# Optimization experiments

Measured on AMD Instinct MI355X. Metric: run time of the kernel, lower is better.

## Reference

```python
import jax, jax.numpy as jnp
import numpy as np

N = 50000   # nodes
E = 800000  # edges (before self-loops)
D = 96      # hidden_dim (= per-head out_channels, concat=False averages heads)
H = 4       # heads
L = 2       # num_layers
NEG_SLOPE = 0.2
EPS_BN = 1e-5


def setup_inputs() -> dict:
    key = jax.random.key(0)
    ks = jax.random.split(key, 8)
    x = jax.random.normal(ks[0], (N, D), dtype=jnp.float32)
    edge_index = jax.random.randint(ks[1], (2, E), 0, N, dtype=jnp.int64)
    # GATConv shared lin: in D -> H*D (per-head dim D), Glorot-ish scale
    W = jax.random.normal(ks[2], (L, D, H * D), dtype=jnp.float32) / np.sqrt(D).astype(np.float32)
    att_src = jax.random.normal(ks[3], (L, H, D), dtype=jnp.float32) * 0.1
    att_dst = jax.random.normal(ks[4], (L, H, D), dtype=jnp.float32) * 0.1
    bias = jnp.zeros((L, D), dtype=jnp.float32)
    gamma = jnp.ones((L, D), dtype=jnp.float32)
    beta = jnp.zeros((L, D), dtype=jnp.float32)
    return dict(x=x, edge_index=edge_index, W=W, att_src=att_src,
                att_dst=att_dst, bias=bias, gamma=gamma, beta=beta)


def _gat_layer(x, src, dst, W, a_src, a_dst, b):
    h = (x @ W).reshape(N, H, D)                      # [N,H,D]
    alpha_src = jnp.einsum('nhd,hd->nh', h, a_src)    # [N,H]
    alpha_dst = jnp.einsum('nhd,hd->nh', h, a_dst)    # [N,H]
    e = jax.nn.leaky_relu(alpha_src[src] + alpha_dst[dst], NEG_SLOPE)  # [Etot,H]
    # edge softmax grouped by destination node (numerically stable)
    m = jax.ops.segment_max(e, dst, num_segments=N)   # [N,H]
    p = jnp.exp(e - m[dst])
    denom = jax.ops.segment_sum(p, dst, num_segments=N)
    alpha = p / (denom[dst] + 1e-16)                  # [Etot,H]
    msg = h[src] * alpha[:, :, None]                  # [Etot,H,D]
    out = jax.ops.segment_sum(msg, dst, num_segments=N)  # [N,H,D]
    return out.mean(axis=1) + b                       # concat=False -> head mean


def reference(x, edge_index, W, att_src, att_dst, bias, gamma, beta):
    # PyG GATConv adds self-loops by default
    loops = jnp.arange(N, dtype=edge_index.dtype)
    ei = jnp.concatenate([edge_index, jnp.stack([loops, loops])], axis=1)
    src, dst = ei[0], ei[1]
    for l in range(L):
        x_res = x
        out = _gat_layer(x, src, dst, W[l], att_src[l], att_dst[l], bias[l])
        # BatchNorm over nodes (training-mode batch statistics, biased var)
        mu = out.mean(axis=0)
        var = out.var(axis=0)
        out = (out - mu) / jnp.sqrt(var + EPS_BN) * gamma[l] + beta[l]
        # dropout is identity at inference
        x = jax.nn.relu(out) + x_res
    return x
```

## Files before the change

### kernel.cpp

```cpp
#include <hip/hip_runtime.h>

#define DD 96
#define HH 4
#define HD 384
#define NEG_SLOPE 0.2f
#define NB_STATS 128
#define SCAN_BS 1024
#define WTC 400

typedef unsigned int uint;
typedef unsigned short ushort;
typedef __attribute__((ext_vector_type(8))) short bf16x8;
typedef __attribute__((ext_vector_type(4))) float f32x4;

__device__ inline uint pack2bf(float lo, float hi) {
    uint ulo = __float_as_uint(lo); ulo += 0x7fffu + ((ulo >> 16) & 1u);
    uint uhi = __float_as_uint(hi); uhi += 0x7fffu + ((uhi >> 16) & 1u);
    return (ulo >> 16) | (uhi & 0xffff0000u);
}
__device__ inline ushort f2bf(float f) {
    uint u = __float_as_uint(f);
    u += 0x7fffu + ((u >> 16) & 1u);
    return (ushort)(u >> 16);
}

__global__ void wa_kernel(const float* __restrict__ W, const float* __restrict__ att_src,
                          const float* __restrict__ att_dst, float* __restrict__ wa) {
    const int l = blockIdx.x / DD;
    const int k = blockIdx.x % DD;
    const int t = threadIdx.x;
    const float* Wr = W + ((size_t)l * DD + k) * HD;
    const float* as = att_src + (size_t)l * HD;
    const float* ad = att_dst + (size_t)l * HD;
    const bool hiHalf = t >= 32;
    float s0=0,s1=0,s2=0,s3=0,d0=0,d1=0,d2=0,d3=0;
    int c; float w, ps, pd;
    c = t;       w = Wr[c]; s0 = fmaf(w, as[c], s0); d0 = fmaf(w, ad[c], d0);
    c = t + 64;  w = Wr[c]; ps = w * as[c]; pd = w * ad[c];
    s0 += hiHalf ? 0.f : ps;  s1 += hiHalf ? ps : 0.f;
    d0 += hiHalf ? 0.f : pd;  d1 += hiHalf ? pd : 0.f;
    c = t + 128; w = Wr[c]; s1 = fmaf(w, as[c], s1); d1 = fmaf(w, ad[c], d1);
    c = t + 192; w = Wr[c]; s2 = fmaf(w, as[c], s2); d2 = fmaf(w, ad[c], d2);
    c = t + 256; w = Wr[c]; ps = w * as[c]; pd = w * ad[c];
    s2 += hiHalf ? 0.f : ps;  s3 += hiHalf ? ps : 0.f;
    d2 += hiHalf ? 0.f : pd;  d3 += hiHalf ? pd : 0.f;
    c = t + 320; w = Wr[c]; s3 = fmaf(w, as[c], s3); d3 = fmaf(w, ad[c], d3);
#pragma unroll
    for (int off = 32; off; off >>= 1) {
        s0 += __shfl_xor(s0, off); s1 += __shfl_xor(s1, off);
        s2 += __shfl_xor(s2, off); s3 += __shfl_xor(s3, off);
        d0 += __shfl_xor(d0, off); d1 += __shfl_xor(d1, off);
        d2 += __shfl_xor(d2, off); d3 += __shfl_xor(d3, off);
    }
    if (t == 0) {
        float* o = wa + ((size_t)l * DD + k) * 8;
        o[0]=s0; o[1]=d0; o[2]=s1; o[3]=d1; o[4]=s2; o[5]=d2; o[6]=s3; o[7]=d3;
    }
}

__global__ void wt_kernel(const float* __restrict__ W, const float* __restrict__ wa,
                          ushort* __restrict__ wt) {
    const int l = blockIdx.x / WTC;
    const int c = blockIdx.x % WTC;
    const int k = threadIdx.x;
    float v = 0.f;
    if (c < HD)        v = W[((size_t)l * DD + k) * HD + c];
    else if (c < HD+8) v = wa[((size_t)l * DD + k) * 8 + (c - HD)];
    wt[((size_t)l * WTC + c) * DD + k] = f2bf(v);
}

template<int FUSE>
__global__ void __launch_bounds__(256) gemm_mfma_kernel(const float* __restrict__ xin,
        const float* __restrict__ scsh, const float* __restrict__ xres,
        float* __restrict__ xout,
        const ushort* __restrict__ wt, uint* __restrict__ hp,
        float* __restrict__ asrc, float* __restrict__ adst, int N) {
    const int t = threadIdx.x;
    const int w = t >> 6;
    const int lane = t & 63;
    const int q = lane & 15, g = lane >> 4;
    const int base = blockIdx.x * 64 + w * 16;
    const int nA = min(base + q, N - 1);

    f32x4 acc[25];
#pragma unroll
    for (int i = 0; i < 25; i++) acc[i] = (f32x4){0.f, 0.f, 0.f, 0.f};

#pragma unroll
    for (int s = 0; s < 3; s++) {
        const int kbase = s * 32 + g * 8;
        float xv[8];
        if (FUSE == 0) {
            const float* xp = xin + (size_t)nA * DD + kbase;
            const float4 xa = *(const float4*)xp;
            const float4 xb = *(const float4*)(xp + 4);
            xv[0]=xa.x; xv[1]=xa.y; xv[2]=xa.z; xv[3]=xa.w;
            xv[4]=xb.x; xv[5]=xb.y; xv[6]=xb.z; xv[7]=xb.w;
        } else {
            const float* yp = xin + (size_t)nA * DD + kbase;
            const float* rp = xres + (size_t)nA * DD + kbase;
            const float4 ya = *(const float4*)yp;
            const float4 yb = *(const float4*)(yp + 4);
            const float4 ra = *(const float4*)rp;
            const float4 rb = *(const float4*)(rp + 4);
            const float yv[8] = {ya.x,ya.y,ya.z,ya.w,yb.x,yb.y,yb.z,yb.w};
            const float rv[8] = {ra.x,ra.y,ra.z,ra.w,rb.x,rb.y,rb.z,rb.w};
#pragma unroll
            for (int j = 0; j < 8; j++) {
                const int d = kbase + j;
                float a = fmaf(yv[j], scsh[d], scsh[d + DD]);
                xv[j] = (a > 0.f ? a : 0.f) + rv[j];
            }
            float* op = xout + (size_t)nA * DD + kbase;
            *(float4*)op       = make_float4(xv[0], xv[1], xv[2], xv[3]);
            *(float4*)(op + 4) = make_float4(xv[4], xv[5], xv[6], xv[7]);
        }
        union { uint u[4]; bf16x8 v; } A;
        A.u[0] = pack2bf(xv[0], xv[1]);
        A.u[1] = pack2bf(xv[2], xv[3]);
        A.u[2] = pack2bf(xv[4], xv[5]);
        A.u[3] = pack2bf(xv[6], xv[7]);
#pragma unroll
        for (int tt = 0; tt < 25; tt++) {
            const ushort* wp = wt + (size_t)(tt * 16 + q) * DD + kbase;
            union { uint4 u4; bf16x8 v; } B;
            B.u4 = *(const uint4*)wp;
            acc[tt] = __builtin_amdgcn_mfma_f32_16x16x32_bf16(A.v, B.v, acc[tt], 0, 0, 0);
        }
    }
#pragma unroll
    for (int r = 0; r < 4; r++) {
        const int node = base + g * 4 + r;
        if (node < N) {
            uint* hr = hp + (size_t)node * 192;
#pragma unroll
            for (int p = 0; p < 3; p++)
#pragma unroll
                for (int tt = 0; tt < 4; tt++)
                    hr[p * 64 + tt * 16 + q] = pack2bf(acc[p * 8 + tt][r], acc[p * 8 + tt + 4][r]);
            if (q < 8) {
                const float v = acc[24][r];
                if ((q & 1) == 0) asrc[node * 4 + (q >> 1)] = v;
                else              adst[node * 4 + (q >> 1)] = v;
            }
        }
    }
}

__global__ void count_kernel(const int* __restrict__ ei, int* __restrict__ deg, int E) {
    int i = blockIdx.x * blockDim.x + threadIdx.x;
    const int stride = gridDim.x * blockDim.x;
    for (; i < E; i += stride) atomicAdd(&deg[ei[E + i]], 1);
}

__global__ void scan1_kernel(const int* __restrict__ deg, int* __restrict__ locpre,
                             int* __restrict__ bsum, int N) {
    __shared__ int ts[256];
    const int t = threadIdx.x;
    const int base = blockIdx.x * SCAN_BS + t * 4;
    int e0 = 0, e1 = 0, e2 = 0, e3 = 0;
    if (base + 3 < N) {
        const int4 v = *(const int4*)(deg + base);
        e0 = v.x + 1; e1 = v.y + 1; e2 = v.z + 1; e3 = v.w + 1;
    } else {
        if (base     < N) e0 = deg[base]     + 1;
        if (base + 1 < N) e1 = deg[base + 1] + 1;
        if (base + 2 < N) e2 = deg[base + 2] + 1;
        if (base + 3 < N) e3 = deg[base + 3] + 1;
    }
    const int s = e0 + e1 + e2 + e3;
    ts[t] = s;
    __syncthreads();
    for (int off = 1; off < 256; off <<= 1) {
        const int u = (t >= off) ? ts[t - off] : 0;
        __syncthreads();
        ts[t] += u;
        __syncthreads();
    }
    const int ex = ts[t] - s;
    if (base + 3 < N) {
        *(int4*)(locpre + base) = make_int4(ex, ex + e0, ex + e0 + e1, ex + e0 + e1 + e2);
    } else if (base < N) {
        locpre[base] = ex;
        if (base + 1 < N) locpre[base + 1] = ex + e0;
        if (base + 2 < N) locpre[base + 2] = ex + e0 + e1;
    }
    if (t == 255) bsum[blockIdx.x] = ts[255];
}

__global__ void scan3_kernel(const int* __restrict__ locpre, const int* __restrict__ bsum,
                             int* __restrict__ rowptr, int* __restrict__ cursor,
                             int N, int NBLK) {
    __shared__ int s_boff, s_total;
    const int t = threadIdx.x;
    if (t < 64) {
        const int mine = (t < NBLK) ? bsum[t] : 0;
        int incl = mine;
#pragma unroll
        for (int off = 1; off < 64; off <<= 1) {
            const int u = __shfl_up(incl, off);
            if (t >= off) incl += u;
        }
        if (t == (int)blockIdx.x) s_boff = incl - mine;
        if (t == NBLK - 1) s_total = incl;
    }
    __syncthreads();
    const int boff = s_boff;
    const int base = blockIdx.x * SCAN_BS + t * 4;
    if (base + 3 < N) {
        int4 v = *(const int4*)(locpre + base);
        v.x += boff; v.y += boff; v.z += boff; v.w += boff;
        *(int4*)(rowptr + base) = v;
        *(int4*)(cursor + base) = v;
    } else {
        for (int i = base; i < N && i < base + 4; i++) {
            const int r = locpre[i] + boff;
            rowptr[i] = r; cursor[i] = r;
        }
    }
    if (blockIdx.x == 0 && t == 0) rowptr[N] = s_total;
}

__global__ void scatter_kernel(const int* __restrict__ ei, int* __restrict__ cursor,
                               const int* __restrict__ rowptr, int* __restrict__ col,
                               int E, int Etot) {
    int i = blockIdx.x * blockDim.x + threadIdx.x;
    const int stride = gridDim.x * blockDim.x;
    for (; i < Etot; i += stride) {
        if (i < E) {
            const int src = ei[i], dst = ei[E + i];
            col[atomicAdd(&cursor[dst], 1)] = src;
        } else {
            const int n = i - E;
            col[rowptr[n + 1] - 1] = n;
        }
    }
}

#define EDGE_FMA(u0, u1, u2, w4)                                                      \
    { den0 += w4.x; den1 += w4.y; den2 += w4.z; den3 += w4.w;                         \
      const float cf1 = hi32 ? w4.y : w4.x;                                           \
      const float cf4 = hi32 ? w4.w : w4.z;                                           \
      acc0 = fmaf(__uint_as_float(u0 << 16), w4.x, acc0);                             \
      acc1 = fmaf(__uint_as_float(u0 & 0xffff0000u), cf1, acc1);                      \
      acc2 = fmaf(__uint_as_float(u1 << 16), w4.y, acc2);                             \
      acc3 = fmaf(__uint_as_float(u1 & 0xffff0000u), w4.z, acc3);                     \
      acc4 = fmaf(__uint_as_float(u2 << 16), cf4, acc4);                              \
      acc5 = fmaf(__uint_as_float(u2 & 0xffff0000u), w4.w, acc5); }

__global__ void __launch_bounds__(256) agg_csr_kernel(
        const int* __restrict__ rowptr, const int* __restrict__ col,
        const uint* __restrict__ hp, const float* __restrict__ asrc,
        const float* __restrict__ adst, const float* __restrict__ bias,
        float* __restrict__ y, int N) {
    __shared__ float4 wls[4][64];
    __shared__ int    sls[4][64];
    const int t = threadIdx.x;
    const int lane = t & 63;
    const int wv = t >> 6;
    const bool hi32 = lane >= 32;
    const int n = (blockIdx.x * blockDim.x + t) >> 6;
    if (n >= N) return;
    const int beg = rowptr[n], endp = rowptr[n + 1];
    const float4 adv = ((const float4*)adst)[n];
    float acc0=0,acc1=0,acc2=0,acc3=0,acc4=0,acc5=0;
    float den0=0,den1=0,den2=0,den3=0;

    for (int cs = beg; cs < endp; cs += 64) {
        const int cnt = min(64, endp - cs);
        if (lane < cnt) {
            const int s = col[cs + lane];
            const float4 av = ((const float4*)asrc)[s];
            float e0 = av.x + adv.x, e1 = av.y + adv.y;
            float e2 = av.z + adv.z, e3 = av.w + adv.w;
            e0 = e0 > 0.f ? e0 : NEG_SLOPE * e0;
            e1 = e1 > 0.f ? e1 : NEG_SLOPE * e1;
            e2 = e2 > 0.f ? e2 : NEG_SLOPE * e2;
            e3 = e3 > 0.f ? e3 : NEG_SLOPE * e3;
            sls[wv][lane] = s;
            wls[wv][lane] = make_float4(__expf(e0), __expf(e1), __expf(e2), __expf(e3));
        }
        __builtin_amdgcn_wave_barrier();
        int j = 0;
        for (; j + 4 <= cnt; j += 4) {
            const int4 sv = *(const int4*)&sls[wv][j];
            const float4 wA = wls[wv][j],     wB = wls[wv][j + 1];
            const float4 wC = wls[wv][j + 2], wD = wls[wv][j + 3];
            const uint* h0 = hp + (size_t)sv.x * 192 + lane;
            const uint* h1 = hp + (size_t)sv.y * 192 + lane;
            const uint* h2 = hp + (size_t)sv.z * 192 + lane;
            const uint* h3 = hp + (size_t)sv.w * 192 + lane;
            const uint u00 = h0[0], u01 = h0[64], u02 = h0[128];
            const uint u10 = h1[0], u11 = h1[64], u12 = h1[128];
            const uint u20 = h2[0], u21 = h2[64], u22 = h2[128];
            const uint u30 = h3[0], u31 = h3[64], u32 = h3[128];
            EDGE_FMA(u00, u01, u02, wA);
            EDGE_FMA(u10, u11, u12, wB);
            EDGE_FMA(u20, u21, u22, wC);
            EDGE_FMA(u30, u31, u32, wD);
        }
        for (; j < cnt; j++) {
            const int s0 = sls[wv][j];
            const float4 wA = wls[wv][j];
            const uint* h0 = hp + (size_t)s0 * 192 + lane;
            const uint u00 = h0[0], u01 = h0[64], u02 = h0[128];
            EDGE_FMA(u00, u01, u02, wA);
        }
        __builtin_amdgcn_wave_barrier();
    }
    const float r0 = 0.25f / (den0 + 1e-16f);
    const float r1 = 0.25f / (den1 + 1e-16f);
    const float r2 = 0.25f / (den2 + 1e-16f);
    const float r3 = 0.25f / (den3 + 1e-16f);
    const float rc1 = hi32 ? r1 : r0;
    const float rc4 = hi32 ? r3 : r2;
    const float A = acc0 * r0 + acc3 * r2;
    const float B = acc1 * rc1 + acc4 * rc4;
    const float C = acc2 * r1 + acc5 * r3;
    const float shB = __shfl_xor(B, 32);
    const float shC = __shfl_xor(C, 32);
    float* yr = y + (size_t)n * DD;
    yr[lane] = A + (hi32 ? shC : shB) + bias[lane];
    if (!hi32) yr[64 + lane] = B + shC + bias[64 + lane];
}

__global__ void bnstats_kernel(const float* __restrict__ y, float* __restrict__ pbuf,
                               int total4) {
    __shared__ float ps[384 * 4];
    __shared__ float qs[384 * 4];
    const int t = threadIdx.x;
    const int stride = gridDim.x * 384;
    float s0=0,s1=0,s2=0,s3=0,q0=0,q1=0,q2=0,q3=0;
    for (int i = blockIdx.x * 384 + t; i < total4; i += stride) {
        const float4 v = ((const float4*)y)[i];
        s0 += v.x; q0 = fmaf(v.x, v.x, q0);
        s1 += v.y; q1 = fmaf(v.y, v.y, q1);
        s2 += v.z; q2 = fmaf(v.z, v.z, q2);
        s3 += v.w; q3 = fmaf(v.w, v.w, q3);
    }
    ps[t*4+0]=s0; ps[t*4+1]=s1; ps[t*4+2]=s2; ps[t*4+3]=s3;
    qs[t*4+0]=q0; qs[t*4+1]=q1; qs[t*4+2]=q2; qs[t*4+3]=q3;
    __syncthreads();
    if (t < 192) {
        const int d = t % 96;
        const float* src = (t < 96) ? ps : qs;
        float r = 0.f;
#pragma unroll
        for (int m = 0; m < 16; m++) r += src[d + 96 * m];
        pbuf[blockIdx.x * 192 + t] = r;
    }
}

__global__ void bnfin_kernel(const float* __restrict__ pbuf, const float* __restrict__ gamma,
                             const float* __restrict__ beta, float* __restrict__ scsh, int N) {
    const int d = threadIdx.x;
    float s = 0.f, q = 0.f;
    for (int b = 0; b < NB_STATS; b++) {
        s += pbuf[b * 192 + d];
        q += pbuf[b * 192 + 96 + d];
    }
    const float invN = 1.f / (float)N;
    const float mu = s * invN;
    const float var = q * invN - mu * mu;
    const float sc = gamma[d] * rsqrtf(var + 1e-5f);
    scsh[d] = sc;
    scsh[d + DD] = beta[d] - mu * sc;
}

__global__ void bn_apply_kernel(const float* __restrict__ y, const float* __restrict__ scsh,
                                const float* __restrict__ xin, float* __restrict__ xout,
                                int total4) {
    int i = blockIdx.x * blockDim.x + threadIdx.x;
    const int stride = gridDim.x * blockDim.x;
    for (; i < total4; i += stride) {
        const int d4 = (i % 24) * 4;
        const float4 v = ((const float4*)y)[i];
        const float4 xi = ((const float4*)xin)[i];
        float4 o; float a;
        a = fmaf(v.x, scsh[d4],     scsh[d4 + DD]);     o.x = (a > 0.f ? a : 0.f) + xi.x;
        a = fmaf(v.y, scsh[d4 + 1], scsh[d4 + 1 + DD]); o.y = (a > 0.f ? a : 0.f) + xi.y;
        a = fmaf(v.z, scsh[d4 + 2], scsh[d4 + 2 + DD]); o.z = (a > 0.f ? a : 0.f) + xi.z;
        a = fmaf(v.w, scsh[d4 + 3], scsh[d4 + 3 + DD]); o.w = (a > 0.f ? a : 0.f) + xi.w;
        ((float4*)xout)[i] = o;
    }
}

extern "C" void kernel_launch(void* const* d_in, const int* in_sizes, int n_in,
                              void* d_out, int out_size, void* d_ws, size_t ws_size,
                              hipStream_t stream) {
    const float* x        = (const float*)d_in[0];
    const int*   ei       = (const int*)d_in[1];
    const float* W        = (const float*)d_in[2];
    const float* att_src  = (const float*)d_in[3];
    const float* att_dst  = (const float*)d_in[4];
    const float* bias     = (const float*)d_in[5];
    const float* gamma    = (const float*)d_in[6];
    const float* beta     = (const float*)d_in[7];
    float* out_final = (float*)d_out;

    const int N = in_sizes[0] / DD;
    const int E = in_sizes[1] / 2;
    const int Etot = E + N;
    const int NBLK = (N + SCAN_BS - 1) / SCAN_BS;

    char* ws = (char*)d_ws;
    size_t off = 0;
    auto alloc = [&](size_t bytes) -> void* {
        void* p = ws + off;
        off += (bytes + 255) & ~(size_t)255;
        return p;
    };
    uint*   hp     = (uint*)alloc((size_t)N * 192 * 4);
    float*  asrc   = (float*)alloc((size_t)N * HH * 4);
    float*  adst   = (float*)alloc((size_t)N * HH * 4);
    float*  y      = (float*)alloc((size_t)N * DD * 4);
    float*  xbuf   = (float*)alloc((size_t)N * DD * 4);
    float*  pbuf   = (float*)alloc((size_t)NB_STATS * 192 * 4);
    float*  scsh   = (float*)alloc(2 * DD * 4);
    float*  wa     = (float*)alloc(2 * DD * 8 * 4);
    ushort* wt     = (ushort*)alloc((size_t)2 * WTC * DD * 2);
    int*    deg    = (int*)alloc((size_t)N * 4);
    int*    locpre = (int*)alloc((size_t)N * 4);
    int*    bsum   = (int*)alloc(64 * 4);
    int*    rowptr = (int*)alloc((size_t)(N + 1) * 4);
    int*    cursor = (int*)alloc((size_t)N * 4);
    int*    colidx = (int*)alloc((size_t)Etot * 4);

    hipMemsetAsync(deg, 0, (size_t)N * 4, stream);
    count_kernel<<<1024, 256, 0, stream>>>(ei, deg, E);
    scan1_kernel<<<NBLK, 256, 0, stream>>>(deg, locpre, bsum, N);
    scan3_kernel<<<NBLK, 256, 0, stream>>>(locpre, bsum, rowptr, cursor, N, NBLK);
    scatter_kernel<<<1024, 256, 0, stream>>>(ei, cursor, rowptr, colidx, E, Etot);
    wa_kernel<<<2 * DD, 64, 0, stream>>>(W, att_src, att_dst, wa);
    wt_kernel<<<2 * WTC, DD, 0, stream>>>(W, wa, wt);

    gemm_mfma_kernel<0><<<(N + 63) / 64, 256, 0, stream>>>(
        x, nullptr, nullptr, nullptr, wt, hp, asrc, adst, N);
    agg_csr_kernel<<<(N * 64 + 255) / 256, 256, 0, stream>>>(
        rowptr, colidx, hp, asrc, adst, bias, y, N);
    bnstats_kernel<<<NB_STATS, 384, 0, stream>>>(y, pbuf, N * DD / 4);
    bnfin_kernel<<<1, DD, 0, stream>>>(pbuf, gamma, beta, scsh, N);

    gemm_mfma_kernel<1><<<(N + 63) / 64, 256, 0, stream>>>(
        y, scsh, x, xbuf, wt + (size_t)WTC * DD, hp, asrc, adst, N);
    agg_csr_kernel<<<(N * 64 + 255) / 256, 256, 0, stream>>>(
        rowptr, colidx, hp, asrc, adst, bias + DD, y, N);
    bnstats_kernel<<<NB_STATS, 384, 0, stream>>>(y, pbuf, N * DD / 4);
    bnfin_kernel<<<1, DD, 0, stream>>>(pbuf, gamma + DD, beta + DD, scsh, N);
    bn_apply_kernel<<<2048, 256, 0, stream>>>(y, scsh, xbuf, out_final, N * DD / 4);
}
```

Baseline: 396.3 us.

## Fuse BatchNorm statistics into aggregation kernel via block-reduced atomics

Each aggregation block reduces per-feature sums and sums of squares in shared memory and atomically adds them to a 192-float global buffer. This replaces the separate bnstats pass that re-read y, and the GEMM kernel zeroes the buffer beforehand. It saves one full read of the output and one launch per layer, at the cost of heavy atomic contention on 192 addresses and a sync in every aggregation block.

```diff
diff --git a/kernel.cpp b/kernel.cpp
--- a/kernel.cpp
+++ b/kernel.cpp
@@ -4,7 +4,6 @@
 #define HH 4
 #define HD 384
 #define NEG_SLOPE 0.2f
-#define NB_STATS 128
 #define SCAN_BS 1024
 #define WTC 400
 
@@ -72,7 +71,7 @@
 template<int FUSE>
 __global__ void __launch_bounds__(256) gemm_mfma_kernel(const float* __restrict__ xin,
         const float* __restrict__ scsh, const float* __restrict__ xres,
-        float* __restrict__ xout,
+        float* __restrict__ xout, float* __restrict__ bnsum,
         const ushort* __restrict__ wt, uint* __restrict__ hp,
         float* __restrict__ asrc, float* __restrict__ adst, int N) {
     const int t = threadIdx.x;
@@ -81,6 +80,7 @@
     const int q = lane & 15, g = lane >> 4;
     const int base = blockIdx.x * 64 + w * 16;
     const int nA = min(base + q, N - 1);
+    if (blockIdx.x == 0 && t < 192) bnsum[t] = 0.f;
 
     f32x4 acc[25];
 #pragma unroll
@@ -252,17 +252,20 @@
         const int* __restrict__ rowptr, const int* __restrict__ col,
         const uint* __restrict__ hp, const float* __restrict__ asrc,
         const float* __restrict__ adst, const float* __restrict__ bias,
-        float* __restrict__ y, int N) {
+        float* __restrict__ y, float* __restrict__ bnsum, int N) {
     __shared__ float4 wls[4][64];
     __shared__ int    sls[4][64];
+    __shared__ float  bsm[4][96];
+    __shared__ float  bsq[4][96];
     const int t = threadIdx.x;
     const int lane = t & 63;
     const int wv = t >> 6;
     const bool hi32 = lane >= 32;
     const int n = (blockIdx.x * blockDim.x + t) >> 6;
-    if (n >= N) return;
-    const int beg = rowptr[n], endp = rowptr[n + 1];
-    const float4 adv = ((const float4*)adst)[n];
+    const bool valid = n < N;
+    int beg = 0, endp = 0;
+    float4 adv = make_float4(0.f, 0.f, 0.f, 0.f);
+    if (valid) { beg = rowptr[n]; endp = rowptr[n + 1]; adv = ((const float4*)adst)[n]; }
     float acc0=0,acc1=0,acc2=0,acc3=0,acc4=0,acc5=0;
     float den0=0,den1=0,den2=0,den3=0;
 
@@ -319,49 +322,38 @@
     const float C = acc2 * r1 + acc5 * r3;
     const float shB = __shfl_xor(B, 32);
     const float shC = __shfl_xor(C, 32);
-    float* yr = y + (size_t)n * DD;
-    yr[lane] = A + (hi32 ? shC : shB) + bias[lane];
-    if (!hi32) yr[64 + lane] = B + shC + bias[64 + lane];
-}
-
-__global__ void bnstats_kernel(const float* __restrict__ y, float* __restrict__ pbuf,
-                               int total4) {
-    __shared__ float ps[384 * 4];
-    __shared__ float qs[384 * 4];
-    const int t = threadIdx.x;
-    const int stride = gridDim.x * 384;
-    float s0=0,s1=0,s2=0,s3=0,q0=0,q1=0,q2=0,q3=0;
-    for (int i = blockIdx.x * 384 + t; i < total4; i += stride) {
-        const float4 v = ((const float4*)y)[i];
-        s0 += v.x; q0 = fmaf(v.x, v.x, q0);
-        s1 += v.y; q1 = fmaf(v.y, v.y, q1);
-        s2 += v.z; q2 = fmaf(v.z, v.z, q2);
-        s3 += v.w; q3 = fmaf(v.w, v.w, q3);
-    }
-    ps[t*4+0]=s0; ps[t*4+1]=s1; ps[t*4+2]=s2; ps[t*4+3]=s3;
-    qs[t*4+0]=q0; qs[t*4+1]=q1; qs[t*4+2]=q2; qs[t*4+3]=q3;
+    float val0 = 0.f, val1 = 0.f;
+    if (valid) {
+        val0 = A + (hi32 ? shC : shB) + bias[lane];
+        val1 = B + shC + bias[64 + lane];
+        float* yr = y + (size_t)n * DD;
+        yr[lane] = val0;
+        if (!hi32) yr[64 + lane] = val1;
+    }
+    bsm[wv][lane] = val0;
+    bsq[wv][lane] = val0 * val0;
+    if (!hi32) {
+        const float v1 = valid ? val1 : 0.f;
+        bsm[wv][64 + lane] = v1;
+        bsq[wv][64 + lane] = v1 * v1;
+    }
     __syncthreads();
-    if (t < 192) {
-        const int d = t % 96;
-        const float* src = (t < 96) ? ps : qs;
-        float r = 0.f;
-#pragma unroll
-        for (int m = 0; m < 16; m++) r += src[d + 96 * m];
-        pbuf[blockIdx.x * 192 + t] = r;
-    }
-}
-
-__global__ void bnfin_kernel(const float* __restrict__ pbuf, const float* __restrict__ gamma,
+    if (t < 96) {
+        const float s = bsm[0][t] + bsm[1][t] + bsm[2][t] + bsm[3][t];
+        unsafeAtomicAdd(&bnsum[t], s);
+    } else if (t < 192) {
+        const int d = t - 96;
+        const float q = bsq[0][d] + bsq[1][d] + bsq[2][d] + bsq[3][d];
+        unsafeAtomicAdd(&bnsum[96 + d], q);
+    }
+}
+
+__global__ void bnfin_kernel(const float* __restrict__ bnsum, const float* __restrict__ gamma,
                              const float* __restrict__ beta, float* __restrict__ scsh, int N) {
     const int d = threadIdx.x;
-    float s = 0.f, q = 0.f;
-    for (int b = 0; b < NB_STATS; b++) {
-        s += pbuf[b * 192 + d];
-        q += pbuf[b * 192 + 96 + d];
-    }
     const float invN = 1.f / (float)N;
-    const float mu = s * invN;
-    const float var = q * invN - mu * mu;
+    const float mu = bnsum[d] * invN;
+    const float var = bnsum[96 + d] * invN - mu * mu;
     const float sc = gamma[d] * rsqrtf(var + 1e-5f);
     scsh[d] = sc;
     scsh[d + DD] = beta[d] - mu * sc;
@@ -415,37 +407,35 @@
     float*  adst   = (float*)alloc((size_t)N * HH * 4);
     float*  y      = (float*)alloc((size_t)N * DD * 4);
     float*  xbuf   = (float*)alloc((size_t)N * DD * 4);
-    float*  pbuf   = (float*)alloc((size_t)NB_STATS * 192 * 4);
+    float*  bnsum  = (float*)alloc(192 * 4);
     float*  scsh   = (float*)alloc(2 * DD * 4);
     float*  wa     = (float*)alloc(2 * DD * 8 * 4);
     ushort* wt     = (ushort*)alloc((size_t)2 * WTC * DD * 2);
     int*    deg    = (int*)alloc((size_t)N * 4);
     int*    locpre = (int*)alloc((size_t)N * 4);
-    int*    bsum   = (int*)alloc(64 * 4);
+    int*    bsumi  = (int*)alloc(64 * 4);
     int*    rowptr = (int*)alloc((size_t)(N + 1) * 4);
     int*    cursor = (int*)alloc((size_t)N * 4);
     int*    colidx = (int*)alloc((size_t)Etot * 4);
 
     hipMemsetAsync(deg, 0, (size_t)N * 4, stream);
     count_kernel<<<1024, 256, 0, stream>>>(ei, deg, E);
-    scan1_kernel<<<NBLK, 256, 0, stream>>>(deg, locpre, bsum, N);
-    scan3_kernel<<<NBLK, 256, 0, stream>>>(locpre, bsum, rowptr, cursor, N, NBLK);
+    scan1_kernel<<<NBLK, 256, 0, stream>>>(deg, locpre, bsumi, N);
+    scan3_kernel<<<NBLK, 256, 0, stream>>>(locpre, bsumi, rowptr, cursor, N, NBLK);
     scatter_kernel<<<1024, 256, 0, stream>>>(ei, cursor, rowptr, colidx, E, Etot);
     wa_kernel<<<2 * DD, 64, 0, stream>>>(W, att_src, att_dst, wa);
     wt_kernel<<<2 * WTC, DD, 0, stream>>>(W, wa, wt);
 
     gemm_mfma_kernel<0><<<(N + 63) / 64, 256, 0, stream>>>(
-        x, nullptr, nullptr, nullptr, wt, hp, asrc, adst, N);
+        x, nullptr, nullptr, nullptr, bnsum, wt, hp, asrc, adst, N);
     agg_csr_kernel<<<(N * 64 + 255) / 256, 256, 0, stream>>>(
-        rowptr, colidx, hp, asrc, adst, bias, y, N);
-    bnstats_kernel<<<NB_STATS, 384, 0, stream>>>(y, pbuf, N * DD / 4);
-    bnfin_kernel<<<1, DD, 0, stream>>>(pbuf, gamma, beta, scsh, N);
+        rowptr, colidx, hp, asrc, adst, bias, y, bnsum, N);
+    bnfin_kernel<<<1, DD, 0, stream>>>(bnsum, gamma, beta, scsh, N);
 
     gemm_mfma_kernel<1><<<(N + 63) / 64, 256, 0, stream>>>(
-        y, scsh, x, xbuf, wt + (size_t)WTC * DD, hp, asrc, adst, N);
+        y, scsh, x, xbuf, bnsum, wt + (size_t)WTC * DD, hp, asrc, adst, N);
     agg_csr_kernel<<<(N * 64 + 255) / 256, 256, 0, stream>>>(
-        rowptr, colidx, hp, asrc, adst, bias + DD, y, N);
-    bnstats_kernel<<<NB_STATS, 384, 0, stream>>>(y, pbuf, N * DD / 4);
-    bnfin_kernel<<<1, DD, 0, stream>>>(pbuf, gamma + DD, beta + DD, scsh, N);
+        rowptr, colidx, hp, asrc, adst, bias + DD, y, bnsum, N);
+    bnfin_kernel<<<1, DD, 0, stream>>>(bnsum, gamma + DD, beta + DD, scsh, N);
     bn_apply_kernel<<<2048, 256, 0, stream>>>(y, scsh, xbuf, out_final, N * DD / 4);
 }
```

New measurement: 811.3 us. 2.05x slower.
